# Optimization experiments

Hardware: AMD Instinct MI355X
Metric: run time of the kernel (lower is better)

The kernel has to match this reference:

```python
import jax, jax.numpy as jnp
import numpy as np

B, N, E = 65536, 5, 8
NF, EF = 7, 2            # raw node/edge feature dims
D, DE = 128, 32          # node/edge embedding dims
L = 4                    # num_convs
PD = 256                 # pool_dim
M1, M2 = 256, 64         # MLP hidden sizes
NEG_SLOPE = 0.01


def lrelu(x):
    return jnp.where(x >= 0, x, NEG_SLOPE * x)


def setup_inputs() -> dict:
    key = jax.random.key(0)
    ks = iter(jax.random.split(key, 40))

    def w(shape, scale=0.05):
        return (jax.random.normal(next(ks), shape, dtype=jnp.float32) * scale)

    inp = {
        "node_feat": jax.random.normal(next(ks), (B, N, NF), dtype=jnp.float32),
        "edge_feat": jax.random.normal(next(ks), (B, E, EF), dtype=jnp.float32),
        "edge_index": jax.random.randint(next(ks), (2, E), 0, N, dtype=jnp.int64),
        "node_w": w((NF, D)), "node_b": jnp.zeros((D,), jnp.float32),
        "edge_w": w((EF, DE)), "edge_b": jnp.zeros((DE,), jnp.float32),
        # stacked per-conv params (L layers)
        "msg_w1": w((L, 2 * D + DE, D)), "msg_b1": jnp.zeros((L, D), jnp.float32),
        "msg_w2": w((L, D, D)), "msg_b2": jnp.zeros((L, D), jnp.float32),
        "upd_w1": w((L, 2 * D, D)), "upd_b1": jnp.zeros((L, D), jnp.float32),
        "upd_g1": jnp.ones((L, N), jnp.float32), "upd_be1": jnp.zeros((L, N), jnp.float32),
        "upd_w2": w((L, D, D)), "upd_b2": jnp.zeros((L, D), jnp.float32),
        "upd_g2": jnp.ones((L, N), jnp.float32), "upd_be2": jnp.zeros((L, N), jnp.float32),
        "pool_w": w((N * D, PD)), "pool_b": jnp.zeros((PD,), jnp.float32),
        "pool_g": jnp.ones((PD,), jnp.float32), "pool_be": jnp.zeros((PD,), jnp.float32),
        "mlp1_w": w((PD, M1)), "mlp1_b": jnp.zeros((M1,), jnp.float32),
        "mlp1_g": jnp.ones((M1,), jnp.float32), "mlp1_be": jnp.zeros((M1,), jnp.float32),
        "mlp2_w": w((M1, M2)), "mlp2_b": jnp.zeros((M2,), jnp.float32),
        "mlp2_g": jnp.ones((M2,), jnp.float32), "mlp2_be": jnp.zeros((M2,), jnp.float32),
    }
    return inp


def _forward(node_feat, edge_feat, edge_index,
             node_w, node_b, edge_w, edge_b,
             msg_w1, msg_b1, msg_w2, msg_b2,
             upd_w1, upd_b1, upd_g1, upd_be1,
             upd_w2, upd_b2, upd_g2, upd_be2,
             pool_w, pool_b, pool_g, pool_be,
             mlp1_w, mlp1_b, mlp1_g, mlp1_be,
             mlp2_w, mlp2_b, mlp2_g, mlp2_be):
    src, dst = edge_index[0], edge_index[1]  # PyG: row0 = j (source), row1 = i (target)
    x = node_feat @ node_w + node_b                    # [B,N,D]
    ea = edge_feat @ edge_w + edge_b                   # [B,E,DE]
    for l in range(L):
        h_i = x[:, dst, :]                             # [B,E,D]
        h_j = x[:, src, :]
        m = jnp.concatenate([h_i, h_j, ea], axis=-1)   # [B,E,2D+DE]
        m = lrelu(m @ msg_w1[l] + msg_b1[l])
        m = lrelu(m @ msg_w2[l] + msg_b2[l])           # [B,E,D]
        agg = jnp.zeros_like(x).at[:, dst, :].add(m)   # scatter-add over nodes
        u = jnp.concatenate([x, agg], axis=-1)         # [B,N,2D]
        u = u @ upd_w1[l] + upd_b1[l]
        u = u * upd_g1[l][None, :, None] + upd_be1[l][None, :, None]  # BatchNorm1d(5), eval
        u = lrelu(u)
        u = u @ upd_w2[l] + upd_b2[l]
        u = u * upd_g2[l][None, :, None] + upd_be2[l][None, :, None]
        u = lrelu(u)
        x = x + u                                      # residual
    p = x.reshape(B, N * D)                            # == cat([x[:,i,:] for i in range(5)])
    p = lrelu((p @ pool_w + pool_b) * pool_g + pool_be)
    p = lrelu((p @ mlp1_w + mlp1_b) * mlp1_g + mlp1_be)
    p = lrelu((p @ mlp2_w + mlp2_b) * mlp2_g + mlp2_be)
    return jnp.mean(p, axis=-1)                        # AvgPool1d over final dim -> [B]


def reference(node_feat, edge_feat, edge_index,
              node_w, node_b, edge_w, edge_b,
              msg_w1, msg_b1, msg_w2, msg_b2,
              upd_w1, upd_b1, upd_g1, upd_be1,
              upd_w2, upd_b2, upd_g2, upd_be2,
              pool_w, pool_b, pool_g, pool_be,
              mlp1_w, mlp1_b, mlp1_g, mlp1_be,
              mlp2_w, mlp2_b, mlp2_g, mlp2_be):
    return _forward(node_feat, edge_feat, edge_index,
                    node_w, node_b, edge_w, edge_b,
                    msg_w1, msg_b1, msg_w2, msg_b2,
                    upd_w1, upd_b1, upd_g1, upd_be1,
                    upd_w2, upd_b2, upd_g2, upd_be2,
                    pool_w, pool_b, pool_g, pool_be,
                    mlp1_w, mlp1_b, mlp1_g, mlp1_be,
                    mlp2_w, mlp2_b, mlp2_g, mlp2_be)
```

## Files before the change

kernel.cpp:

```cpp
#include <hip/hip_runtime.h>


typedef _Float16 h8 __attribute__((ext_vector_type(8)));
typedef float f4 __attribute__((ext_vector_type(4)));

constexpr int NB = 65536;
constexpr int GG = 16;
constexpr int NBLK = NB / GG;

__device__ __forceinline__ float lrelu(float v){ return v >= 0.f ? v : 0.01f*v; }
__device__ __forceinline__ int div5(int v){ return (v*52429)>>18; }

__device__ __forceinline__ _Float16* sw8(_Float16* b, int row, int offh){
    int byte = (row<<8) + (offh<<1);
    byte ^= (row&7)<<4;
    return (_Float16*)((char*)b + byte);
}
__device__ __forceinline__ _Float16* swea(_Float16* b, int row, int offh){
    int byte = (row<<6) + (offh<<1);
    byte ^= (row&3)<<4;
    return (_Float16*)((char*)b + byte);
}

#define MFMA(a,b,c) __builtin_amdgcn_mfma_f32_16x16x32_f16((a),(b),(c),0,0,0)

__device__ __forceinline__ f4 z4(){ f4 v; v[0]=0.f; v[1]=0.f; v[2]=0.f; v[3]=0.f; return v; }

__global__ void prep_t(const float* __restrict__ src, _Float16* __restrict__ dst,
                       int K, int N, int total){
    int i = blockIdx.x*256 + threadIdx.x;
    if (i >= total) return;
    int kn = K*N;
    int l = i / kn; int r = i - l*kn;
    int n = r / K;  int k = r - n*K;
    dst[i] = (_Float16)src[(size_t)l*kn + (size_t)k*N + n];
}

constexpr int O_MSG1 = 0;
constexpr int O_MSG2 = 147456;
constexpr int O_UPD1 = 212992;
constexpr int O_UPD2 = 344064;
constexpr int O_POOL = 409600;
constexpr int O_MLP1 = 573440;
constexpr int O_MLP2 = 638976;

__global__ __launch_bounds__(512) __attribute__((amdgpu_waves_per_eu(4, 4)))
void gnn_mfma(const float* __restrict__ nfeat, const float* __restrict__ efeat,
              const int* __restrict__ eidx,
              const float* __restrict__ node_w, const float* __restrict__ node_b,
              const float* __restrict__ edge_w, const float* __restrict__ edge_b,
              const _Float16* __restrict__ wT,
              const float* __restrict__ msg_b1, const float* __restrict__ msg_b2,
              const float* __restrict__ upd_b1, const float* __restrict__ upd_g1, const float* __restrict__ upd_be1,
              const float* __restrict__ upd_b2, const float* __restrict__ upd_g2, const float* __restrict__ upd_be2,
              const float* __restrict__ pool_b, const float* __restrict__ pool_g, const float* __restrict__ pool_be,
              const float* __restrict__ mlp1_b, const float* __restrict__ mlp1_g, const float* __restrict__ mlp1_be,
              const float* __restrict__ mlp2_b, const float* __restrict__ mlp2_g, const float* __restrict__ mlp2_be,
              float* __restrict__ out)
{
    extern __shared__ char smem[];
    _Float16* xh  = (_Float16*)(smem);
    _Float16* ea  = (_Float16*)(smem + 20480);
    _Float16* buf = (_Float16*)(smem + 28672);
    _Float16* agg = (_Float16*)(smem + 61440);
    float*    miscf = (float*)(smem + 61440);
    float*    partf = (float*)(smem + 61440);

    const int tid  = threadIdx.x;
    const int w    = tid >> 6;
    const int lane = tid & 63;
    const int l15  = lane & 15;
    const int kg   = lane >> 4;
    const int mgM  = w >> 1;
    const int ngM  = w & 1;
    const int mgU  = w >> 1;
    const int cntU = (mgU < 2) ? 2 : ((mgU == 2) ? 1 : 0);
    const int gbase = blockIdx.x * GG;

    int dp = 0, sp = 0;
    {
        bool is64 = true;
        #pragma unroll
        for (int i = 1; i < 16; i += 2) if (eidx[i] != 0) is64 = false;
        #pragma unroll
        for (int e = 0; e < 8; ++e){
            int s = is64 ? eidx[2*e]     : eidx[e];
            int d = is64 ? eidx[16+2*e]  : eidx[8+e];
            sp |= s << (4*e); dp |= d << (4*e);
        }
    }
    const int eMine = l15 & 7;
    const int myDst = (dp >> (4*eMine)) & 15;
    const int mySrc = (sp >> (4*eMine)) & 15;

    for (int i = tid; i < 816; i += 512){
        if (i < 560) miscf[i] = nfeat[(size_t)gbase*35 + i];
        else         miscf[i] = efeat[(size_t)gbase*16 + (i - 560)];
    }
    __syncthreads();

    {
        int u  = tid;
        int ge = u >> 2, c8 = (u & 3) * 8;
        int g  = ge >> 3, e = ge & 7;
        float f0 = miscf[560 + g*16 + e*2];
        float f1 = miscf[560 + g*16 + e*2 + 1];
        h8 v;
        #pragma unroll
        for (int j = 0; j < 8; ++j){
            int c = c8 + j;
            v[j] = (_Float16)(edge_b[c] + f0*edge_w[c] + f1*edge_w[32 + c]);
        }
        *(h8*)swea(ea, ge, c8) = v;
    }

    float xreg[2][4][4];
    #pragma unroll
    for (int mi = 0; mi < 2; ++mi){
        if (mi < cntU){
            int mt = mgU*2 + mi;
            #pragma unroll
            for (int nt = 0; nt < 4; ++nt){
                int col = ngM*64 + nt*16 + l15;
                float w0 = node_w[0*128+col], w1 = node_w[1*128+col],
                      w2 = node_w[2*128+col], w3 = node_w[3*128+col],
                      w4 = node_w[4*128+col], w5 = node_w[5*128+col],
                      w6 = node_w[6*128+col];
                float bb = node_b[col];
                #pragma unroll
                for (int r = 0; r < 4; ++r){
                    int row = mt*16 + kg*4 + r;
                    int g = div5(row), n = row - 5*g;
                    const float* nf = &miscf[g*35 + n*7];
                    float v = bb + nf[0]*w0 + nf[1]*w1 + nf[2]*w2 + nf[3]*w3
                                 + nf[4]*w4 + nf[5]*w5 + nf[6]*w6;
                    xreg[mi][nt][r] = v;
                    *sw8(xh, row, col) = (_Float16)v;
                }
            }
        }
    }
    __syncthreads();

    for (int l = 0; l < 4; ++l){
        const _Float16* W1 = wT + O_MSG1 + (size_t)l*36864;
        const _Float16* W2 = wT + O_MSG2 + (size_t)l*16384;
        const _Float16* W3 = wT + O_UPD1 + (size_t)l*32768;
        const _Float16* W4 = wT + O_UPD2 + (size_t)l*16384;

        {
            f4 acc[2][4];
            #pragma unroll
            for (int mi=0;mi<2;++mi){ acc[mi][0]=z4(); acc[mi][1]=z4(); acc[mi][2]=z4(); acc[mi][3]=z4(); }
            int xrow_d[2], xrow_s[2], earow[2];
            #pragma unroll
            for (int mi = 0; mi < 2; ++mi){
                int mt = mgM*2 + mi;
                int g  = mt*2 + (l15 >> 3);
                xrow_d[mi] = g*5 + myDst;
                xrow_s[mi] = g*5 + mySrc;
                earow[mi]  = mt*16 + l15;
            }
            const _Float16* Bp = W1 + (size_t)(ngM*64 + l15)*288 + kg*8;
            #pragma unroll
            for (int kc = 0; kc < 4; ++kc){
                h8 a0 = *(const h8*)sw8(xh, xrow_d[0], kc*32 + kg*8);
                h8 a1 = *(const h8*)sw8(xh, xrow_d[1], kc*32 + kg*8);
                #pragma unroll
                for (int np = 0; np < 2; ++np){
                    h8 b0 = *(const h8*)(Bp + (2*np+0)*4608 + kc*32);
                    h8 b1 = *(const h8*)(Bp + (2*np+1)*4608 + kc*32);
                    acc[0][2*np]=MFMA(a0,b0,acc[0][2*np]); acc[0][2*np+1]=MFMA(a0,b1,acc[0][2*np+1]);
                    acc[1][2*np]=MFMA(a1,b0,acc[1][2*np]); acc[1][2*np+1]=MFMA(a1,b1,acc[1][2*np+1]);
                }
            }
            #pragma unroll
            for (int kc = 0; kc < 4; ++kc){
                h8 a0 = *(const h8*)sw8(xh, xrow_s[0], kc*32 + kg*8);
                h8 a1 = *(const h8*)sw8(xh, xrow_s[1], kc*32 + kg*8);
                #pragma unroll
                for (int np = 0; np < 2; ++np){
                    h8 b0 = *(const h8*)(Bp + (2*np+0)*4608 + 128 + kc*32);
                    h8 b1 = *(const h8*)(Bp + (2*np+1)*4608 + 128 + kc*32);
                    acc[0][2*np]=MFMA(a0,b0,acc[0][2*np]); acc[0][2*np+1]=MFMA(a0,b1,acc[0][2*np+1]);
                    acc[1][2*np]=MFMA(a1,b0,acc[1][2*np]); acc[1][2*np+1]=MFMA(a1,b1,acc[1][2*np+1]);
                }
            }
            {
                h8 a0 = *(const h8*)swea(ea, earow[0], kg*8);
                h8 a1 = *(const h8*)swea(ea, earow[1], kg*8);
                #pragma unroll
                for (int np = 0; np < 2; ++np){
                    h8 b0 = *(const h8*)(Bp + (2*np+0)*4608 + 256);
                    h8 b1 = *(const h8*)(Bp + (2*np+1)*4608 + 256);
                    acc[0][2*np]=MFMA(a0,b0,acc[0][2*np]); acc[0][2*np+1]=MFMA(a0,b1,acc[0][2*np+1]);
                    acc[1][2*np]=MFMA(a1,b0,acc[1][2*np]); acc[1][2*np+1]=MFMA(a1,b1,acc[1][2*np+1]);
                }
            }
            #pragma unroll
            for (int mi = 0; mi < 2; ++mi){
                int mt = mgM*2 + mi;
                #pragma unroll
                for (int nt = 0; nt < 4; ++nt){
                    int col = ngM*64 + nt*16 + l15;
                    float bb = msg_b1[l*128 + col];
                    #pragma unroll
                    for (int r = 0; r < 4; ++r){
                        int row = mt*16 + kg*4 + r;
                        *sw8(buf, row, col) = (_Float16)lrelu(acc[mi][nt][r] + bb);
                    }
                }
            }
        }
        __syncthreads();

        {
            f4 acc[2][4];
            #pragma unroll
            for (int mi=0;mi<2;++mi){ acc[mi][0]=z4(); acc[mi][1]=z4(); acc[mi][2]=z4(); acc[mi][3]=z4(); }
            const _Float16* Bp = W2 + (size_t)(ngM*64 + l15)*128 + kg*8;
            #pragma unroll
            for (int kc = 0; kc < 4; ++kc){
                h8 a0 = *(const h8*)sw8(buf, (mgM*2+0)*16 + l15, kc*32 + kg*8);
                h8 a1 = *(const h8*)sw8(buf, (mgM*2+1)*16 + l15, kc*32 + kg*8);
                #pragma unroll
                for (int np = 0; np < 2; ++np){
                    h8 b0 = *(const h8*)(Bp + (2*np+0)*2048 + kc*32);
                    h8 b1 = *(const h8*)(Bp + (2*np+1)*2048 + kc*32);
                    acc[0][2*np]=MFMA(a0,b0,acc[0][2*np]); acc[0][2*np+1]=MFMA(a0,b1,acc[0][2*np+1]);
                    acc[1][2*np]=MFMA(a1,b0,acc[1][2*np]); acc[1][2*np+1]=MFMA(a1,b1,acc[1][2*np+1]);
                }
            }
            __syncthreads();
            #pragma unroll
            for (int mi = 0; mi < 2; ++mi){
                int mt = mgM*2 + mi;
                #pragma unroll
                for (int nt = 0; nt < 4; ++nt){
                    int col = ngM*64 + nt*16 + l15;
                    float bb = msg_b2[l*128 + col];
                    #pragma unroll
                    for (int r = 0; r < 4; ++r){
                        int row = mt*16 + kg*4 + r;
                        *sw8(buf, row, col) = (_Float16)lrelu(acc[mi][nt][r] + bb);
                    }
                }
            }
        }
        __syncthreads();

        for (int u = tid; u < 1280; u += 512){
            int gn = u >> 4, c8 = (u & 15)*8;
            int g = div5(gn), n = gn - 5*g;
            float s0=0,s1=0,s2=0,s3=0,s4=0,s5=0,s6=0,s7=0;
            #pragma unroll
            for (int e = 0; e < 8; ++e){
                if (((dp >> (4*e)) & 15) == n){
                    h8 v = *(const h8*)sw8(buf, g*8 + e, c8);
                    s0+=(float)v[0]; s1+=(float)v[1]; s2+=(float)v[2]; s3+=(float)v[3];
                    s4+=(float)v[4]; s5+=(float)v[5]; s6+=(float)v[6]; s7+=(float)v[7];
                }
            }
            h8 o;
            o[0]=(_Float16)s0; o[1]=(_Float16)s1; o[2]=(_Float16)s2; o[3]=(_Float16)s3;
            o[4]=(_Float16)s4; o[5]=(_Float16)s5; o[6]=(_Float16)s6; o[7]=(_Float16)s7;
            *(h8*)sw8(agg, gn, c8) = o;
        }
        __syncthreads();

        if (cntU > 0){
            f4 acc[2][4];
            #pragma unroll
            for (int mi=0;mi<2;++mi){ acc[mi][0]=z4(); acc[mi][1]=z4(); acc[mi][2]=z4(); acc[mi][3]=z4(); }
            const _Float16* Bp = W3 + (size_t)(ngM*64 + l15)*256 + kg*8;
            #pragma unroll
            for (int kc = 0; kc < 8; ++kc){
                h8 a0, a1;
                if (kc < 4) { a0 = *(const h8*)sw8(xh,  (mgU*2+0)*16 + l15, kc*32 + kg*8); }
                else        { a0 = *(const h8*)sw8(agg, (mgU*2+0)*16 + l15, (kc-4)*32 + kg*8); }
                if (cntU > 1){
                    if (kc < 4) { a1 = *(const h8*)sw8(xh,  (mgU*2+1)*16 + l15, kc*32 + kg*8); }
                    else        { a1 = *(const h8*)sw8(agg, (mgU*2+1)*16 + l15, (kc-4)*32 + kg*8); }
                } else a1 = a0;
                #pragma unroll
                for (int np = 0; np < 2; ++np){
                    h8 b0 = *(const h8*)(Bp + (2*np+0)*4096 + kc*32);
                    h8 b1 = *(const h8*)(Bp + (2*np+1)*4096 + kc*32);
                    acc[0][2*np]=MFMA(a0,b0,acc[0][2*np]); acc[0][2*np+1]=MFMA(a0,b1,acc[0][2*np+1]);
                    if (cntU > 1){
                        acc[1][2*np]=MFMA(a1,b0,acc[1][2*np]); acc[1][2*np+1]=MFMA(a1,b1,acc[1][2*np+1]);
                    }
                }
            }
            #pragma unroll
            for (int mi = 0; mi < 2; ++mi){
                if (mi < cntU){
                    int mt = mgU*2 + mi;
                    #pragma unroll
                    for (int nt = 0; nt < 4; ++nt){
                        int col = ngM*64 + nt*16 + l15;
                        float bb = upd_b1[l*128 + col];
                        #pragma unroll
                        for (int r = 0; r < 4; ++r){
                            int crow = mt*16 + kg*4 + r;
                            int n = crow - 5*div5(crow);
                            float val = lrelu((acc[mi][nt][r] + bb)*upd_g1[l*5+n] + upd_be1[l*5+n]);
                            *sw8(buf, crow, col) = (_Float16)val;
                        }
                    }
                }
            }
        }
        __syncthreads();

        if (cntU > 0){
            f4 acc[2][4];
            #pragma unroll
            for (int mi=0;mi<2;++mi){ acc[mi][0]=z4(); acc[mi][1]=z4(); acc[mi][2]=z4(); acc[mi][3]=z4(); }
            const _Float16* Bp = W4 + (size_t)(ngM*64 + l15)*128 + kg*8;
            #pragma unroll
            for (int kc = 0; kc < 4; ++kc){
                h8 a0 = *(const h8*)sw8(buf, (mgU*2+0)*16 + l15, kc*32 + kg*8);
                h8 a1 = (cntU > 1) ? *(const h8*)sw8(buf, (mgU*2+1)*16 + l15, kc*32 + kg*8) : a0;
                #pragma unroll
                for (int np = 0; np < 2; ++np){
                    h8 b0 = *(const h8*)(Bp + (2*np+0)*2048 + kc*32);
                    h8 b1 = *(const h8*)(Bp + (2*np+1)*2048 + kc*32);
                    acc[0][2*np]=MFMA(a0,b0,acc[0][2*np]); acc[0][2*np+1]=MFMA(a0,b1,acc[0][2*np+1]);
                    if (cntU > 1){
                        acc[1][2*np]=MFMA(a1,b0,acc[1][2*np]); acc[1][2*np+1]=MFMA(a1,b1,acc[1][2*np+1]);
                    }
                }
            }
            #pragma unroll
            for (int mi = 0; mi < 2; ++mi){
                if (mi < cntU){
                    int mt = mgU*2 + mi;
                    #pragma unroll
                    for (int nt = 0; nt < 4; ++nt){
                        int col = ngM*64 + nt*16 + l15;
                        float bb = upd_b2[l*128 + col];
                        #pragma unroll
                        for (int r = 0; r < 4; ++r){
                            int crow = mt*16 + kg*4 + r;
                            int n = crow - 5*div5(crow);
                            float val = lrelu((acc[mi][nt][r] + bb)*upd_g2[l*5+n] + upd_be2[l*5+n]);
                            xreg[mi][nt][r] += val;
                            *sw8(xh, crow, col) = (_Float16)xreg[mi][nt][r];
                        }
                    }
                }
            }
        }
        __syncthreads();
    }

    {
        f4 accP[2]; accP[0]=z4(); accP[1]=z4();
        const _Float16* Bp = wT + O_POOL + (size_t)(w*32 + l15)*640 + kg*8;
        #pragma unroll
        for (int kc = 0; kc < 20; ++kc){
            int k0 = kc*32 + kg*8;
            int n  = k0 >> 7, d = k0 & 127;
            h8 a  = *(const h8*)sw8(xh, l15*5 + n, d);
            h8 b0 = *(const h8*)(Bp + kc*32);
            h8 b1 = *(const h8*)(Bp + 16*640 + kc*32);
            accP[0]=MFMA(a,b0,accP[0]); accP[1]=MFMA(a,b1,accP[1]);
        }
        #pragma unroll
        for (int nt = 0; nt < 2; ++nt){
            int col = w*32 + nt*16 + l15;
            float pb = pool_b[col], pg = pool_g[col], pe = pool_be[col];
            #pragma unroll
            for (int r = 0; r < 4; ++r){
                int g = kg*4 + r;
                float val = lrelu((accP[nt][r] + pb)*pg + pe);
                int prow = g + 16*(col >> 7);
                *sw8(buf, prow, col & 127) = (_Float16)val;
            }
        }
    }
    __syncthreads();

    {
        f4 accQ[2]; accQ[0]=z4(); accQ[1]=z4();
        const _Float16* Bp = wT + O_MLP1 + (size_t)(w*32 + l15)*256 + kg*8;
        #pragma unroll
        for (int kc = 0; kc < 8; ++kc){
            int k0 = kc*32 + kg*8;
            int arow = l15 + 16*(k0 >> 7);
            h8 a  = *(const h8*)sw8(buf, arow, k0 & 127);
            h8 b0 = *(const h8*)(Bp + kc*32);
            h8 b1 = *(const h8*)(Bp + 16*256 + kc*32);
            accQ[0]=MFMA(a,b0,accQ[0]); accQ[1]=MFMA(a,b1,accQ[1]);
        }
        __syncthreads();
        #pragma unroll
        for (int nt = 0; nt < 2; ++nt){
            int col = w*32 + nt*16 + l15;
            float qb = mlp1_b[col], qg = mlp1_g[col], qe = mlp1_be[col];
            #pragma unroll
            for (int r = 0; r < 4; ++r){
                int g = kg*4 + r;
                float val = lrelu((accQ[nt][r] + qb)*qg + qe);
                int qrow = 32 + g + 16*(col >> 7);
                *sw8(buf, qrow, col & 127) = (_Float16)val;
            }
        }
    }
    __syncthreads();

    if (w < 4){
        f4 accR = z4();
        const _Float16* Bp = wT + O_MLP2 + (size_t)(w*16 + l15)*256 + kg*8;
        #pragma unroll
        for (int kc = 0; kc < 8; ++kc){
            int k0 = kc*32 + kg*8;
            int arow = 32 + l15 + 16*(k0 >> 7);
            h8 a = *(const h8*)sw8(buf, arow, k0 & 127);
            h8 b = *(const h8*)(Bp + kc*32);
            accR = MFMA(a, b, accR);
        }
        int col = w*16 + l15;
        float rb = mlp2_b[col], rg = mlp2_g[col], re = mlp2_be[col];
        #pragma unroll
        for (int r = 0; r < 4; ++r){
            float val = lrelu((accR[r] + rb)*rg + re);
            val += __shfl_xor(val, 1);
            val += __shfl_xor(val, 2);
            val += __shfl_xor(val, 4);
            val += __shfl_xor(val, 8);
            if (l15 == 0) partf[w*16 + (kg*4 + r)] = val;
        }
    }
    __syncthreads();
    if (tid < 16){
        float s = partf[tid] + partf[16+tid] + partf[32+tid] + partf[48+tid];
        out[gbase + tid] = s * (1.0f/64.0f);
    }
}

extern "C" void kernel_launch(void* const* d_in, const int* in_sizes, int n_in,
                              void* d_out, int out_size, void* d_ws, size_t ws_size,
                              hipStream_t stream) {
    _Float16* wT = (_Float16*)d_ws;
    auto T = [&](const void* src, int dstoff, int L, int K, int N){
        int total = L*K*N;
        prep_t<<<(total + 255)/256, 256, 0, stream>>>((const float*)src, wT + dstoff, K, N, total);
    };
    T(d_in[7],  O_MSG1, 4, 288, 128);
    T(d_in[9],  O_MSG2, 4, 128, 128);
    T(d_in[11], O_UPD1, 4, 256, 128);
    T(d_in[15], O_UPD2, 4, 128, 128);
    T(d_in[19], O_POOL, 1, 640, 256);
    T(d_in[23], O_MLP1, 1, 256, 256);
    T(d_in[27], O_MLP2, 1, 256, 64);

    gnn_mfma<<<NBLK, 512, 81920, stream>>>(
        (const float*)d_in[0], (const float*)d_in[1], (const int*)d_in[2],
        (const float*)d_in[3], (const float*)d_in[4],
        (const float*)d_in[5], (const float*)d_in[6],
        wT,
        (const float*)d_in[8],  (const float*)d_in[10],
        (const float*)d_in[12], (const float*)d_in[13], (const float*)d_in[14],
        (const float*)d_in[16], (const float*)d_in[17], (const float*)d_in[18],
        (const float*)d_in[20], (const float*)d_in[21], (const float*)d_in[22],
        (const float*)d_in[24], (const float*)d_in[25], (const float*)d_in[26],
        (const float*)d_in[28], (const float*)d_in[29], (const float*)d_in[30],
        (float*)d_out);
}
```

Before: 2.047 ms.

## Halve graphs per block to 8 with 256 threads and static smaller LDS

Each block now processes 8 graphs with 256 threads instead of 16 graphs with 512, and uses a static 44KB LDS layout instead of 80KB dynamic. The per-wave work in the message, update, pool and MLP stages is re-split, and rows beyond the 40 real node rows are masked. The intent is higher occupancy and less LDS pressure per block. In exchange, MFMA tiles are now partly padded: rows 8-15 hold duplicate or unused data in the pool and MLP GEMMs, and M-tiles exceed 40 rows in the update GEMMs. This wastes matrix throughput and doubles the number of per-block weight reads.

New measurement: 2.182 ms. +6.6%, slower.

```diff
diff --git a/kernel.cpp b/kernel.cpp
--- a/kernel.cpp
+++ b/kernel.cpp
@@ -5,21 +5,21 @@
 typedef float f4 __attribute__((ext_vector_type(4)));
 
 constexpr int NB = 65536;
-constexpr int GG = 16;
+constexpr int GG = 8;
 constexpr int NBLK = NB / GG;
 
 __device__ __forceinline__ float lrelu(float v){ return v >= 0.f ? v : 0.01f*v; }
 __device__ __forceinline__ int div5(int v){ return (v*52429)>>18; }
 
-__device__ __forceinline__ _Float16* sw8(_Float16* b, int row, int offh){
+__device__ __forceinline__ _Float16* sw8(char* base, int row, int offh){
     int byte = (row<<8) + (offh<<1);
     byte ^= (row&7)<<4;
-    return (_Float16*)((char*)b + byte);
+    return (_Float16*)(base + byte);
 }
-__device__ __forceinline__ _Float16* swea(_Float16* b, int row, int offh){
+__device__ __forceinline__ _Float16* swea(char* base, int row, int offh){
     int byte = (row<<6) + (offh<<1);
     byte ^= (row&3)<<4;
-    return (_Float16*)((char*)b + byte);
+    return (_Float16*)(base + byte);
 }
 
 #define MFMA(a,b,c) __builtin_amdgcn_mfma_f32_16x16x32_f16((a),(b),(c),0,0,0)
@@ -44,7 +44,13 @@
 constexpr int O_MLP1 = 573440;
 constexpr int O_MLP2 = 638976;
 
-__global__ __launch_bounds__(512) __attribute__((amdgpu_waves_per_eu(4, 4)))
+constexpr int LO_XH  = 0;
+constexpr int LO_EA  = 12288;
+constexpr int LO_BUF = 16384;
+constexpr int LO_AGG = 32768;
+constexpr int LDS_BYTES = 45056;
+
+__global__ __launch_bounds__(256)
 void gnn_mfma(const float* __restrict__ nfeat, const float* __restrict__ efeat,
               const int* __restrict__ eidx,
               const float* __restrict__ node_w, const float* __restrict__ node_b,
@@ -58,13 +64,13 @@
               const float* __restrict__ mlp2_b, const float* __restrict__ mlp2_g, const float* __restrict__ mlp2_be,
               float* __restrict__ out)
 {
-    extern __shared__ char smem[];
-    _Float16* xh  = (_Float16*)(smem);
-    _Float16* ea  = (_Float16*)(smem + 20480);
-    _Float16* buf = (_Float16*)(smem + 28672);
-    _Float16* agg = (_Float16*)(smem + 61440);
-    float*    miscf = (float*)(smem + 61440);
-    float*    partf = (float*)(smem + 61440);
+    __shared__ __align__(16) char smem[LDS_BYTES];
+    char* xh  = smem + LO_XH;
+    char* ea  = smem + LO_EA;
+    char* buf = smem + LO_BUF;
+    char* agg = smem + LO_AGG;
+    float* miscf = (float*)(smem + LO_AGG);
+    float* partf = (float*)(smem + LO_AGG);
 
     const int tid  = threadIdx.x;
     const int w    = tid >> 6;
@@ -74,7 +80,7 @@
     const int mgM  = w >> 1;
     const int ngM  = w & 1;
     const int mgU  = w >> 1;
-    const int cntU = (mgU < 2) ? 2 : ((mgU == 2) ? 1 : 0);
+    const int cntU = (mgU == 0) ? 2 : 1;
     const int gbase = blockIdx.x * GG;
 
     int dp = 0, sp = 0;
@@ -93,18 +99,17 @@
     const int myDst = (dp >> (4*eMine)) & 15;
     const int mySrc = (sp >> (4*eMine)) & 15;
 
-    for (int i = tid; i < 816; i += 512){
-        if (i < 560) miscf[i] = nfeat[(size_t)gbase*35 + i];
-        else         miscf[i] = efeat[(size_t)gbase*16 + (i - 560)];
+    for (int i = tid; i < 408; i += 256){
+        if (i < 280) miscf[i] = nfeat[(size_t)gbase*35 + i];
+        else         miscf[i] = efeat[(size_t)gbase*16 + (i - 280)];
     }
     __syncthreads();
 
     {
-        int u  = tid;
-        int ge = u >> 2, c8 = (u & 3) * 8;
+        int ge = tid >> 2, c8 = (tid & 3) * 8;
         int g  = ge >> 3, e = ge & 7;
-        float f0 = miscf[560 + g*16 + e*2];
-        float f1 = miscf[560 + g*16 + e*2 + 1];
+        float f0 = miscf[280 + g*16 + e*2];
+        float f1 = miscf[280 + g*16 + e*2 + 1];
         h8 v;
         #pragma unroll
         for (int j = 0; j < 8; ++j){
@@ -135,7 +140,7 @@
                     float v = bb + nf[0]*w0 + nf[1]*w1 + nf[2]*w2 + nf[3]*w3
                                  + nf[4]*w4 + nf[5]*w5 + nf[6]*w6;
                     xreg[mi][nt][r] = v;
-                    *sw8(xh, row, col) = (_Float16)v;
+                    if (row < 40) *sw8(xh, row, col) = (_Float16)v;
                 }
             }
         }
@@ -249,7 +254,7 @@
         }
         __syncthreads();
 
-        for (int u = tid; u < 1280; u += 512){
+        for (int u = tid; u < 640; u += 256){
             int gn = u >> 4, c8 = (u & 15)*8;
             int g = div5(gn), n = gn - 5*g;
             float s0=0,s1=0,s2=0,s3=0,s4=0,s5=0,s6=0,s7=0;
@@ -268,7 +273,7 @@
         }
         __syncthreads();
 
-        if (cntU > 0){
+        {
             f4 acc[2][4];
             #pragma unroll
             for (int mi=0;mi<2;++mi){ acc[mi][0]=z4(); acc[mi][1]=z4(); acc[mi][2]=z4(); acc[mi][3]=z4(); }
@@ -303,9 +308,11 @@
                         #pragma unroll
                         for (int r = 0; r < 4; ++r){
                             int crow = mt*16 + kg*4 + r;
-                            int n = crow - 5*div5(crow);
-                            float val = lrelu((acc[mi][nt][r] + bb)*upd_g1[l*5+n] + upd_be1[l*5+n]);
-                            *sw8(buf, crow, col) = (_Float16)val;
+                            if (crow < 40){
+                                int n = crow - 5*div5(crow);
+                                float val = lrelu((acc[mi][nt][r] + bb)*upd_g1[l*5+n] + upd_be1[l*5+n]);
+                                *sw8(buf, crow, col) = (_Float16)val;
+                            }
                         }
                     }
                 }
@@ -313,7 +320,7 @@
         }
         __syncthreads();
 
-        if (cntU > 0){
+        {
             f4 acc[2][4];
             #pragma unroll
             for (int mi=0;mi<2;++mi){ acc[mi][0]=z4(); acc[mi][1]=z4(); acc[mi][2]=z4(); acc[mi][3]=z4(); }
@@ -346,7 +353,7 @@
                             int n = crow - 5*div5(crow);
                             float val = lrelu((acc[mi][nt][r] + bb)*upd_g2[l*5+n] + upd_be2[l*5+n]);
                             xreg[mi][nt][r] += val;
-                            *sw8(xh, crow, col) = (_Float16)xreg[mi][nt][r];
+                            if (crow < 40) *sw8(xh, crow, col) = (_Float16)xreg[mi][nt][r];
                         }
                     }
                 }
@@ -356,67 +363,79 @@
     }
 
     {
-        f4 accP[2]; accP[0]=z4(); accP[1]=z4();
-        const _Float16* Bp = wT + O_POOL + (size_t)(w*32 + l15)*640 + kg*8;
+        f4 accP[4];
+        #pragma unroll
+        for (int nt=0;nt<4;++nt) accP[nt]=z4();
+        const _Float16* Bp = wT + O_POOL + (size_t)(w*64 + l15)*640 + kg*8;
         #pragma unroll
         for (int kc = 0; kc < 20; ++kc){
             int k0 = kc*32 + kg*8;
             int n  = k0 >> 7, d = k0 & 127;
-            h8 a  = *(const h8*)sw8(xh, l15*5 + n, d);
-            h8 b0 = *(const h8*)(Bp + kc*32);
-            h8 b1 = *(const h8*)(Bp + 16*640 + kc*32);
-            accP[0]=MFMA(a,b0,accP[0]); accP[1]=MFMA(a,b1,accP[1]);
-        }
-        #pragma unroll
-        for (int nt = 0; nt < 2; ++nt){
-            int col = w*32 + nt*16 + l15;
+            h8 a  = *(const h8*)sw8(xh, (l15 & 7)*5 + n, d);
+            #pragma unroll
+            for (int nt = 0; nt < 4; ++nt){
+                h8 b = *(const h8*)(Bp + nt*10240 + kc*32);
+                accP[nt] = MFMA(a, b, accP[nt]);
+            }
+        }
+        #pragma unroll
+        for (int nt = 0; nt < 4; ++nt){
+            int col = w*64 + nt*16 + l15;
             float pb = pool_b[col], pg = pool_g[col], pe = pool_be[col];
             #pragma unroll
             for (int r = 0; r < 4; ++r){
                 int g = kg*4 + r;
-                float val = lrelu((accP[nt][r] + pb)*pg + pe);
-                int prow = g + 16*(col >> 7);
-                *sw8(buf, prow, col & 127) = (_Float16)val;
+                if (g < 8){
+                    float val = lrelu((accP[nt][r] + pb)*pg + pe);
+                    int prow = g + 16*(col >> 7);
+                    *sw8(buf, prow, col & 127) = (_Float16)val;
+                }
             }
         }
     }
     __syncthreads();
 
     {
-        f4 accQ[2]; accQ[0]=z4(); accQ[1]=z4();
-        const _Float16* Bp = wT + O_MLP1 + (size_t)(w*32 + l15)*256 + kg*8;
+        f4 accQ[4];
+        #pragma unroll
+        for (int nt=0;nt<4;++nt) accQ[nt]=z4();
+        const _Float16* Bp = wT + O_MLP1 + (size_t)(w*64 + l15)*256 + kg*8;
         #pragma unroll
         for (int kc = 0; kc < 8; ++kc){
             int k0 = kc*32 + kg*8;
-            int arow = l15 + 16*(k0 >> 7);
-            h8 a  = *(const h8*)sw8(buf, arow, k0 & 127);
-            h8 b0 = *(const h8*)(Bp + kc*32);
-            h8 b1 = *(const h8*)(Bp + 16*256 + kc*32);
-            accQ[0]=MFMA(a,b0,accQ[0]); accQ[1]=MFMA(a,b1,accQ[1]);
-        }
-        __syncthreads();
-        #pragma unroll
-        for (int nt = 0; nt < 2; ++nt){
-            int col = w*32 + nt*16 + l15;
+            int arow = (l15 & 7) + 16*(k0 >> 7);
+            h8 a = *(const h8*)sw8(buf, arow, k0 & 127);
+            #pragma unroll
+            for (int nt = 0; nt < 4; ++nt){
+                h8 b = *(const h8*)(Bp + nt*4096 + kc*32);
+                accQ[nt] = MFMA(a, b, accQ[nt]);
+            }
+        }
+        __syncthreads();
+        #pragma unroll
+        for (int nt = 0; nt < 4; ++nt){
+            int col = w*64 + nt*16 + l15;
             float qb = mlp1_b[col], qg = mlp1_g[col], qe = mlp1_be[col];
             #pragma unroll
             for (int r = 0; r < 4; ++r){
                 int g = kg*4 + r;
-                float val = lrelu((accQ[nt][r] + qb)*qg + qe);
-                int qrow = 32 + g + 16*(col >> 7);
-                *sw8(buf, qrow, col & 127) = (_Float16)val;
+                if (g < 8){
+                    float val = lrelu((accQ[nt][r] + qb)*qg + qe);
+                    int qrow = 32 + g + 16*(col >> 7);
+                    *sw8(buf, qrow, col & 127) = (_Float16)val;
+                }
             }
         }
     }
     __syncthreads();
 
-    if (w < 4){
+    {
         f4 accR = z4();
         const _Float16* Bp = wT + O_MLP2 + (size_t)(w*16 + l15)*256 + kg*8;
         #pragma unroll
         for (int kc = 0; kc < 8; ++kc){
             int k0 = kc*32 + kg*8;
-            int arow = 32 + l15 + 16*(k0 >> 7);
+            int arow = 32 + (l15 & 7) + 16*(k0 >> 7);
             h8 a = *(const h8*)sw8(buf, arow, k0 & 127);
             h8 b = *(const h8*)(Bp + kc*32);
             accR = MFMA(a, b, accR);
@@ -434,7 +453,7 @@
         }
     }
     __syncthreads();
-    if (tid < 16){
+    if (tid < 8){
         float s = partf[tid] + partf[16+tid] + partf[32+tid] + partf[48+tid];
         out[gbase + tid] = s * (1.0f/64.0f);
     }
@@ -456,7 +475,7 @@
     T(d_in[23], O_MLP1, 1, 256, 256);
     T(d_in[27], O_MLP2, 1, 256, 64);
 
-    gnn_mfma<<<NBLK, 512, 81920, stream>>>(
+    gnn_mfma<<<NBLK, 256, 0, stream>>>(
         (const float*)d_in[0], (const float*)d_in[1], (const int*)d_in[2],
         (const float*)d_in[3], (const float*)d_in[4],
         (const float*)d_in[5], (const float*)d_in[6],
```
